# Kernel optimization log

Measured on AMD Instinct MI355X. Metric: run time of the kernel, lower is better.

Reference implementation:

```python
import jax, jax.numpy as jnp
import numpy as np

DIM = 1024
NUM_HEADS = 16
HEAD_DIM = DIM // NUM_HEADS
GATE_HID = DIM // 4


def setup_inputs() -> dict:
    key = jax.random.key(0)
    ks = jax.random.split(key, 16)
    B, S, D = 2, 2048, DIM
    sc = 1.0 / np.sqrt(D)
    inp = {
        "h": jax.random.normal(ks[0], (B, S, D), jnp.float32),
        "x": jax.random.normal(ks[1], (B, S, D), jnp.float32),
        # attention projections, stored (in, out) so y = x @ W + b
        "Wq": jax.random.normal(ks[2], (D, D), jnp.float32) * sc,
        "bq": jnp.zeros((D,), jnp.float32),
        "Wk": jax.random.normal(ks[3], (D, D), jnp.float32) * sc,
        "bk": jnp.zeros((D,), jnp.float32),
        "Wv": jax.random.normal(ks[4], (D, D), jnp.float32) * sc,
        "bv": jnp.zeros((D,), jnp.float32),
        "Wo": jax.random.normal(ks[5], (D, D), jnp.float32) * sc,
        "bo": jnp.zeros((D,), jnp.float32),
        # gating MLP: Linear(2D -> D//4) -> GELU -> Linear(D//4 -> D) -> sigmoid
        "Wg1": jax.random.normal(ks[6], (2 * D, GATE_HID), jnp.float32) * (1.0 / np.sqrt(2 * D)),
        "bg1": jnp.zeros((GATE_HID,), jnp.float32),
        "Wg2": jax.random.normal(ks[7], (GATE_HID, D), jnp.float32) * (1.0 / np.sqrt(GATE_HID)),
        "bg2": jnp.zeros((D,), jnp.float32),
    }
    return inp


def reference(h, x, Wq, bq, Wk, bk, Wv, bv, Wo, bo, Wg1, bg1, Wg2, bg2):
    B, S, D = h.shape
    # gated blend of latent h and input x
    gate_in = jnp.concatenate([h, x], axis=-1)                      # (B,S,2D)
    gate = jax.nn.sigmoid((jax.nn.gelu(gate_in @ Wg1 + bg1, approximate=False)) @ Wg2 + bg2)
    blended = gate * h + (1.0 - gate) * x                           # (B,S,D)
    # multi-head self-attention
    q = (blended @ Wq + bq).reshape(B, S, NUM_HEADS, HEAD_DIM)
    k = (blended @ Wk + bk).reshape(B, S, NUM_HEADS, HEAD_DIM)
    v = (blended @ Wv + bv).reshape(B, S, NUM_HEADS, HEAD_DIM)
    scale = 1.0 / np.sqrt(HEAD_DIM).astype(np.float32)
    scores = jnp.einsum('bqhd,bkhd->bhqk', q, k) * scale            # (B,H,S,S)
    attn = jax.nn.softmax(scores, axis=-1)
    out = jnp.einsum('bhqk,bkhd->bqhd', attn, v).reshape(B, S, D)
    return out @ Wo + bo
```

## Files before the change

### kernel.cpp

```cpp
#include <hip/hip_runtime.h>
#include <hip/hip_bf16.h>


typedef __attribute__((ext_vector_type(4))) unsigned int u32x4;
typedef __attribute__((ext_vector_type(2))) unsigned int u32x2;
typedef __attribute__((ext_vector_type(8))) short s16x8;
typedef __attribute__((ext_vector_type(8))) unsigned short u16x8;
typedef __attribute__((ext_vector_type(4))) unsigned short u16x4;
typedef __attribute__((ext_vector_type(4))) float f32x4;

#define QSCALE 0.18033688011112043f
#define FIXED_M 24.0f

__device__ __forceinline__ unsigned short f2bf(float f) {
    unsigned int i = __builtin_bit_cast(unsigned int, f) + 0x8000u;
    return (unsigned short)(i >> 16);
}
__device__ __forceinline__ unsigned int pack2bf(float a, float b) {
    unsigned int ia = __builtin_bit_cast(unsigned int, a) + 0x8000u;
    unsigned int ib = __builtin_bit_cast(unsigned int, b) + 0x8000u;
    return __builtin_amdgcn_perm(ib, ia, 0x07060302u);
}

__device__ __forceinline__ void gload16(const void* g, void* l) {
    __builtin_amdgcn_global_load_lds(
        (const __attribute__((address_space(1))) void*)g,
        (__attribute__((address_space(3))) void*)l, 16, 0, 0);
}

struct TEntry { const float* src; unsigned short* dst; int K; int N; };
struct TTable { TEntry e[6]; };

__global__ __launch_bounds__(256) void prep_all(
    TTable tt,
    const float* __restrict__ bq, const float* __restrict__ bk,
    const float* __restrict__ bv, float* __restrict__ bqkv)
{
    const int bid = (int)blockIdx.x;
    const int tid = threadIdx.x;
    if (bid < 3072) {
        const TEntry E = tt.e[bid >> 9];
        const int bx = bid & 511;
        const int ntn = E.N >> 5;
        if (bx >= (E.K >> 6) * ntn) return;
        const int n0 = (bx % ntn) * 32, k0 = (bx / ntn) * 64;
        __shared__ float tile[64][33];
        const int lnn = tid & 31, lkk = tid >> 5;
#pragma unroll
        for (int i = 0; i < 8; ++i)
            tile[lkk + i * 8][lnn] = E.src[(size_t)(k0 + lkk + i * 8) * E.N + n0 + lnn];
        __syncthreads();
        const int snn = tid >> 3, skk = (tid & 7) * 8;
        u16x8 o;
#pragma unroll
        for (int j = 0; j < 8; ++j) o[j] = f2bf(tile[skk + j][snn]);
        *reinterpret_cast<u16x8*>(&E.dst[(size_t)(n0 + snn) * E.K + k0 + skk]) = o;
        return;
    }
    const int i = (bid - 3072) * 256 + tid;
    if (i < 1024) bqkv[i] = bq[i];
    else if (i < 2048) bqkv[i] = bk[i - 1024];
    else if (i < 3072) bqkv[i] = bv[i - 2048];
}

__global__ __launch_bounds__(256) void transpose_v(
    const unsigned short* __restrict__ qkv, unsigned short* __restrict__ vt)
{
    __shared__ unsigned short t[64][65];
    const int st = blockIdx.x;
    const int bh = blockIdx.y;
    const int b = bh >> 4, h = bh & 15;
    const int tx = threadIdx.x & 63, ty = threadIdx.x >> 6;
    const int s0 = st * 64;
    const size_t base = (size_t)(b * 2048 + s0) * 3072 + 2048 + h * 64;
#pragma unroll
    for (int i = 0; i < 16; ++i)
        t[ty + i * 4][tx] = qkv[base + (size_t)(ty + i * 4) * 3072 + tx];
    __syncthreads();
    const size_t obase = (size_t)(bh * 64) * 2048 + s0;
#pragma unroll
    for (int i = 0; i < 16; ++i)
        vt[obase + (size_t)(ty + i * 4) * 2048 + tx] = t[tx][ty + i * 4];
}

enum { EPI_GELU = 1, EPI_BLEND = 2, EPI_F32 = 3, EPI_QKV = 4 };

template <int EPI>
__global__ __launch_bounds__(256, 3) void gemm_kernel(
    const unsigned short* __restrict__ A, int lda,
    const unsigned short* __restrict__ Bt, int ldb,
    const float* __restrict__ bias,
    void* __restrict__ Cv, int ldc, int K,
    const float* __restrict__ hb, const float* __restrict__ xb,
    int swzn, int ntn)
{
    __shared__ unsigned short Alds[2][128 * 32];
    __shared__ unsigned short Blds[2][128 * 32];

    const int tid = threadIdx.x;
    const int lane = tid & 63;
    const int w = tid >> 6;
    const int wr = w >> 1, wc = w & 1;
    int mt, nt;
    if (swzn > 0) {
        const int xcd = (int)blockIdx.x & 7, seq = (int)blockIdx.x >> 3;
        nt = xcd * swzn + seq % swzn;
        mt = seq / swzn;
    } else {
        nt = (int)blockIdx.x % ntn;
        mt = (int)blockIdx.x / ntn;
    }
    const int m0 = mt * 128, n0 = nt * 128;
    const int lrow = lane & 15, lko = (lane >> 4) * 8;

    const int grow = w * 32 + (lane >> 2);
    const int gk8 = (lane & 3) * 8;
    const unsigned short* ga0 = A + (size_t)(m0 + grow) * lda + gk8;
    const unsigned short* ga1 = ga0 + (size_t)16 * lda;
    const unsigned short* gb0 = Bt + (size_t)(n0 + grow) * ldb + gk8;
    const unsigned short* gb1 = gb0 + (size_t)16 * ldb;

    auto stage = [&](int buf, int k0) {
        unsigned short* la = &Alds[buf][w * 1024];
        unsigned short* lb = &Blds[buf][w * 1024];
        gload16(ga0 + k0, la);
        gload16(ga1 + k0, la + 512);
        gload16(gb0 + k0, lb);
        gload16(gb1 + k0, lb + 512);
    };

    f32x4 acc[4][4];
#pragma unroll
    for (int i = 0; i < 4; ++i)
#pragma unroll
        for (int j = 0; j < 4; ++j) acc[i][j] = (f32x4){0.f, 0.f, 0.f, 0.f};

    const int kks = K >> 5;
    stage(0, 0);
    __syncthreads();

    for (int t = 0; t < kks; ++t) {
        const int cur = t & 1;
        if (t + 1 < kks) stage(cur ^ 1, (t + 1) << 5);

        s16x8 af[4], bfr[4];
#pragma unroll
        for (int mi = 0; mi < 4; ++mi)
            af[mi] = *reinterpret_cast<const s16x8*>(&Alds[cur][(wr * 64 + mi * 16 + lrow) * 32 + lko]);
#pragma unroll
        for (int ni = 0; ni < 4; ++ni)
            bfr[ni] = *reinterpret_cast<const s16x8*>(&Blds[cur][(wc * 64 + ni * 16 + lrow) * 32 + lko]);
#pragma unroll
        for (int mi = 0; mi < 4; ++mi)
#pragma unroll
            for (int ni = 0; ni < 4; ++ni)
                acc[mi][ni] = __builtin_amdgcn_mfma_f32_16x16x32_bf16(af[mi], bfr[ni], acc[mi][ni], 0, 0, 0);

        __syncthreads();
    }

    const int rbase = m0 + wr * 64;
    const int cbase = n0 + wc * 64;
#pragma unroll
    for (int mi = 0; mi < 4; ++mi) {
#pragma unroll
        for (int j = 0; j < 4; ++j) {
            const int r = rbase + mi * 16 + (lane >> 4) * 4 + j;
#pragma unroll
            for (int ni = 0; ni < 4; ++ni) {
                const int c = cbase + ni * 16 + (lane & 15);
                float v = acc[mi][ni][j] + bias[c];
                if constexpr (EPI == EPI_GELU) {
                    float g = 0.5f * v * (1.f + erff(v * 0.70710678118654752f));
                    ((unsigned short*)Cv)[(size_t)r * ldc + c] = f2bf(g);
                } else if constexpr (EPI == EPI_BLEND) {
                    float gate = 1.f / (1.f + __expf(-v));
                    const size_t o = (size_t)r * ldc + c;
                    float bl = gate * hb[o] + (1.f - gate) * xb[o];
                    ((unsigned short*)Cv)[o] = f2bf(bl);
                } else if constexpr (EPI == EPI_QKV) {
                    const float scl = (c < 1024) ? QSCALE : 1.f;
                    ((unsigned short*)Cv)[(size_t)r * ldc + c] = f2bf(v * scl);
                } else {
                    ((float*)Cv)[(size_t)r * ldc + c] = v;
                }
            }
        }
    }
}

template <int EPI>
__global__ __launch_bounds__(256, 4) void gemm64_kernel(
    const unsigned short* __restrict__ A, int lda,
    const unsigned short* __restrict__ Bt, int ldb,
    const float* __restrict__ bias,
    void* __restrict__ Cv, int ldc, int K,
    const float* __restrict__ hb, const float* __restrict__ xb,
    int swzn)
{
    __shared__ unsigned short Alds[2][64 * 32];
    __shared__ unsigned short Blds[2][64 * 32];

    const int tid = threadIdx.x;
    const int lane = tid & 63;
    const int w = tid >> 6;
    const int wr = w >> 1, wc = w & 1;
    const int xcd = (int)blockIdx.x & 7, seq = (int)blockIdx.x >> 3;
    const int nt = xcd * swzn + seq % swzn;
    const int mt = seq / swzn;
    const int m0 = mt * 64, n0 = nt * 64;
    const int lrow = lane & 15, lko = (lane >> 4) * 8;

    const int grow = w * 16 + (lane >> 2);
    const int gk8 = (lane & 3) * 8;
    const unsigned short* ga = A + (size_t)(m0 + grow) * lda + gk8;
    const unsigned short* gb = Bt + (size_t)(n0 + grow) * ldb + gk8;

    auto stage = [&](int buf, int k0) {
        gload16(ga + k0, &Alds[buf][w * 512]);
        gload16(gb + k0, &Blds[buf][w * 512]);
    };

    f32x4 acc[2][2];
#pragma unroll
    for (int i = 0; i < 2; ++i)
#pragma unroll
        for (int j = 0; j < 2; ++j) acc[i][j] = (f32x4){0.f, 0.f, 0.f, 0.f};

    const int kks = K >> 5;
    stage(0, 0);
    __syncthreads();

    for (int t = 0; t < kks; ++t) {
        const int cur = t & 1;
        if (t + 1 < kks) stage(cur ^ 1, (t + 1) << 5);

        s16x8 af[2], bfr[2];
#pragma unroll
        for (int mi = 0; mi < 2; ++mi)
            af[mi] = *reinterpret_cast<const s16x8*>(&Alds[cur][(wr * 32 + mi * 16 + lrow) * 32 + lko]);
#pragma unroll
        for (int ni = 0; ni < 2; ++ni)
            bfr[ni] = *reinterpret_cast<const s16x8*>(&Blds[cur][(wc * 32 + ni * 16 + lrow) * 32 + lko]);
#pragma unroll
        for (int mi = 0; mi < 2; ++mi)
#pragma unroll
            for (int ni = 0; ni < 2; ++ni)
                acc[mi][ni] = __builtin_amdgcn_mfma_f32_16x16x32_bf16(af[mi], bfr[ni], acc[mi][ni], 0, 0, 0);

        __syncthreads();
    }

    const int rbase = m0 + wr * 32;
    const int cbase = n0 + wc * 32;
#pragma unroll
    for (int mi = 0; mi < 2; ++mi) {
#pragma unroll
        for (int j = 0; j < 4; ++j) {
            const int r = rbase + mi * 16 + (lane >> 4) * 4 + j;
#pragma unroll
            for (int ni = 0; ni < 2; ++ni) {
                const int c = cbase + ni * 16 + (lane & 15);
                float v = acc[mi][ni][j] + bias[c];
                if constexpr (EPI == EPI_BLEND) {
                    float gate = 1.f / (1.f + __expf(-v));
                    const size_t o = (size_t)r * ldc + c;
                    float bl = gate * hb[o] + (1.f - gate) * xb[o];
                    ((unsigned short*)Cv)[o] = f2bf(bl);
                } else {
                    ((float*)Cv)[(size_t)r * ldc + c] = v;
                }
            }
        }
    }
}

__global__ __launch_bounds__(256, 4) void gelu_partial(
    const float* __restrict__ h, const float* __restrict__ x,
    const unsigned short* __restrict__ Bt,
    float* __restrict__ partial)
{
    __shared__ unsigned short Alds[2][32 * 32];
    __shared__ unsigned short Blds[2][256 * 32];

    const int tid = threadIdx.x;
    const int lane = tid & 63;
    const int w = tid >> 6;
    const int mt = (int)blockIdx.x >> 2, ks = (int)blockIdx.x & 3;
    const int m0 = mt * 32, kbase = ks * 512;
    const int lrow = lane & 15, lko = (lane >> 4) * 8;

    const int arl = tid >> 3, ac4 = (tid & 7) * 4;
    const size_t arg = (size_t)(m0 + arl) * 1024;
    auto loadA = [&](int k0, f32x4& v) {
        v = *reinterpret_cast<const f32x4*>((k0 < 1024 ? h : x) + arg + (k0 & 1023) + ac4);
    };
    auto writeA = [&](int buf, const f32x4& v) {
        u32x2 p = {pack2bf(v[0], v[1]), pack2bf(v[2], v[3])};
        *reinterpret_cast<u32x2*>(&Alds[buf][arl * 32 + ac4]) = p;
    };

    const int brow = w * 64 + (lane >> 2);
    const int bk8 = (lane & 3) * 8;
    const unsigned short* gb = Bt + (size_t)brow * 2048 + kbase + bk8;
    auto stageB = [&](int buf, int k0) {
#pragma unroll
        for (int i = 0; i < 4; ++i)
            gload16(gb + (size_t)(i * 16) * 2048 + k0, &Blds[buf][(w * 64 + i * 16) * 32]);
    };

    f32x4 acc[2][4];
#pragma unroll
    for (int i = 0; i < 2; ++i)
#pragma unroll
        for (int j = 0; j < 4; ++j) acc[i][j] = (f32x4){0.f, 0.f, 0.f, 0.f};

    f32x4 areg;
    loadA(kbase, areg);
    stageB(0, 0);
    writeA(0, areg);
    __syncthreads();

    for (int t = 0; t < 16; ++t) {
        const int cur = t & 1;
        if (t + 1 < 16) {
            loadA(kbase + ((t + 1) << 5), areg);
            stageB(cur ^ 1, (t + 1) << 5);
        }

        s16x8 af[2], bfr[4];
#pragma unroll
        for (int mi = 0; mi < 2; ++mi)
            af[mi] = *reinterpret_cast<const s16x8*>(&Alds[cur][(mi * 16 + lrow) * 32 + lko]);
#pragma unroll
        for (int ni = 0; ni < 4; ++ni)
            bfr[ni] = *reinterpret_cast<const s16x8*>(&Blds[cur][(w * 64 + ni * 16 + lrow) * 32 + lko]);
#pragma unroll
        for (int mi = 0; mi < 2; ++mi)
#pragma unroll
            for (int ni = 0; ni < 4; ++ni)
                acc[mi][ni] = __builtin_amdgcn_mfma_f32_16x16x32_bf16(af[mi], bfr[ni], acc[mi][ni], 0, 0, 0);

        if (t + 1 < 16) writeA(cur ^ 1, areg);
        __syncthreads();
    }

    float* pbase = partial + (size_t)ks * 4096 * 256;
#pragma unroll
    for (int mi = 0; mi < 2; ++mi) {
#pragma unroll
        for (int j = 0; j < 4; ++j) {
            const int r = m0 + mi * 16 + (lane >> 4) * 4 + j;
#pragma unroll
            for (int ni = 0; ni < 4; ++ni) {
                const int c = w * 64 + ni * 16 + (lane & 15);
                pbase[(size_t)r * 256 + c] = acc[mi][ni][j];
            }
        }
    }
}

__global__ __launch_bounds__(256) void gelu_reduce(
    const float* __restrict__ partial, const float* __restrict__ bias,
    unsigned short* __restrict__ g1)
{
    const size_t idx = ((size_t)blockIdx.x * 256 + threadIdx.x) * 4;
    const int c = (int)(idx & 255);
    f32x4 s = *reinterpret_cast<const f32x4*>(partial + idx);
#pragma unroll
    for (int ks = 1; ks < 4; ++ks) {
        f32x4 p = *reinterpret_cast<const f32x4*>(partial + (size_t)ks * 4096 * 256 + idx);
        s[0] += p[0]; s[1] += p[1]; s[2] += p[2]; s[3] += p[3];
    }
    f32x4 bb = *reinterpret_cast<const f32x4*>(bias + c);
    u16x4 o;
#pragma unroll
    for (int j = 0; j < 4; ++j) {
        float v = s[j] + bb[j];
        o[j] = f2bf(0.5f * v * (1.f + erff(v * 0.70710678118654752f)));
    }
    *reinterpret_cast<u16x4*>(g1 + idx) = o;
}

#define ALD 72

__global__ __launch_bounds__(256, 3) void attn_kernel(
    const unsigned short* __restrict__ qkv,
    const unsigned short* __restrict__ vt,
    unsigned short* __restrict__ out)
{
    __shared__ unsigned short Klds[2][64 * 64];
    __shared__ unsigned short Vlds[2][64 * 64];
    __shared__ unsigned short Plds[2][4][16 * ALD];

    const int tid = threadIdx.x, lane = tid & 63, w = tid >> 6;
    const int xcd = (int)blockIdx.x & 7, seq = (int)blockIdx.x >> 3;
    const int bh = xcd * 4 + (seq & 3);
    const int qt = seq >> 2;
    const int b = bh >> 4, h = bh & 15;
    const int rb = b * 2048;
    const int lrow = lane & 15, g = lane >> 4, lko = g * 8;

    s16x8 qf[2][2];
#pragma unroll
    for (int qg = 0; qg < 2; ++qg) {
        const size_t qrow = (size_t)(rb + qt * 128 + w * 32 + qg * 16 + lrow) * 3072 + h * 64;
        qf[qg][0] = *reinterpret_cast<const s16x8*>(qkv + qrow + lko);
        qf[qg][1] = *reinterpret_cast<const s16x8*>(qkv + qrow + 32 + lko);
    }

    const int grow = w * 16 + (lane >> 3);
    const int gswz = ((lane & 7) ^ (lane >> 3)) * 8;
    const unsigned short* kgp = qkv + (size_t)(rb + grow) * 3072 + 1024 + h * 64 + gswz;
    const unsigned short* vgp = vt + (size_t)(bh * 64 + grow) * 2048 + gswz;

    auto stage = [&](int buf, int t0) {
        gload16(kgp + (size_t)t0 * 3072, &Klds[buf][w * 1024]);
        gload16(kgp + (size_t)(t0 + 8) * 3072, &Klds[buf][w * 1024 + 512]);
        gload16(vgp + t0, &Vlds[buf][w * 1024]);
        gload16(vgp + t0 + 8 * 2048, &Vlds[buf][w * 1024 + 512]);
    };

    const int cs0 = ((g) ^ (lrow & 7)) * 8;
    const int cs1 = ((4 + g) ^ (lrow & 7)) * 8;

    f32x4 acc0[4], acc1[4];
#pragma unroll
    for (int di = 0; di < 4; ++di) {
        acc0[di] = (f32x4){0.f, 0.f, 0.f, 0.f};
        acc1[di] = (f32x4){0.f, 0.f, 0.f, 0.f};
    }
    float lsum0 = 0.f, lsum1 = 0.f;

    unsigned short* pw0 = &Plds[0][w][0];
    unsigned short* pw1 = &Plds[1][w][0];
    s16x8 vf[2][4];

    stage(0, 0);
    __syncthreads();

    for (int t0 = 0; t0 < 2048; t0 += 64) {
        const int cur = (t0 >> 6) & 1;
        if (t0 + 64 < 2048) stage(cur ^ 1, t0 + 64);

        if (t0 > 0) {
            __builtin_amdgcn_s_setprio(1);
#pragma unroll
            for (int st = 0; st < 2; ++st) {
                s16x8 pf0 = *reinterpret_cast<const s16x8*>(&pw0[lrow * ALD + st * 32 + lko]);
#pragma unroll
                for (int di = 0; di < 4; ++di)
                    acc0[di] = __builtin_amdgcn_mfma_f32_16x16x32_bf16(vf[st][di], pf0, acc0[di], 0, 0, 0);
            }
#pragma unroll
            for (int st = 0; st < 2; ++st) {
                s16x8 pf1 = *reinterpret_cast<const s16x8*>(&pw1[lrow * ALD + st * 32 + lko]);
#pragma unroll
                for (int di = 0; di < 4; ++di)
                    acc1[di] = __builtin_amdgcn_mfma_f32_16x16x32_bf16(vf[st][di], pf1, acc1[di], 0, 0, 0);
            }
            __builtin_amdgcn_s_setprio(0);
        }

        s16x8 kf[4][2];
#pragma unroll
        for (int ni = 0; ni < 4; ++ni) {
            kf[ni][0] = *reinterpret_cast<const s16x8*>(&Klds[cur][(ni * 16 + lrow) * 64 + cs0]);
            kf[ni][1] = *reinterpret_cast<const s16x8*>(&Klds[cur][(ni * 16 + lrow) * 64 + cs1]);
        }

        f32x4 s0[4];
#pragma unroll
        for (int ni = 0; ni < 4; ++ni)
            s0[ni] = (f32x4){-FIXED_M, -FIXED_M, -FIXED_M, -FIXED_M};
        __builtin_amdgcn_s_setprio(1);
#pragma unroll
        for (int ni = 0; ni < 4; ++ni)
#pragma unroll
            for (int fi = 0; fi < 2; ++fi)
                s0[ni] = __builtin_amdgcn_mfma_f32_16x16x32_bf16(kf[ni][fi], qf[0][fi], s0[ni], 0, 0, 0);
        __builtin_amdgcn_s_setprio(0);

#pragma unroll
        for (int ni = 0; ni < 4; ++ni) {
            float p0 = __builtin_amdgcn_exp2f(s0[ni][0]);
            float p1 = __builtin_amdgcn_exp2f(s0[ni][1]);
            float p2 = __builtin_amdgcn_exp2f(s0[ni][2]);
            float p3 = __builtin_amdgcn_exp2f(s0[ni][3]);
            lsum0 += (p0 + p1) + (p2 + p3);
            u32x2 pk = {pack2bf(p0, p1), pack2bf(p2, p3)};
            *reinterpret_cast<u32x2*>(&pw0[lrow * ALD + ni * 16 + g * 4]) = pk;
        }

        f32x4 s1[4];
#pragma unroll
        for (int ni = 0; ni < 4; ++ni)
            s1[ni] = (f32x4){-FIXED_M, -FIXED_M, -FIXED_M, -FIXED_M};
        __builtin_amdgcn_s_setprio(1);
#pragma unroll
        for (int ni = 0; ni < 4; ++ni)
#pragma unroll
            for (int fi = 0; fi < 2; ++fi)
                s1[ni] = __builtin_amdgcn_mfma_f32_16x16x32_bf16(kf[ni][fi], qf[1][fi], s1[ni], 0, 0, 0);
        __builtin_amdgcn_s_setprio(0);

#pragma unroll
        for (int di = 0; di < 4; ++di) {
            vf[0][di] = *reinterpret_cast<const s16x8*>(&Vlds[cur][(di * 16 + lrow) * 64 + cs0]);
            vf[1][di] = *reinterpret_cast<const s16x8*>(&Vlds[cur][(di * 16 + lrow) * 64 + cs1]);
        }

#pragma unroll
        for (int ni = 0; ni < 4; ++ni) {
            float p0 = __builtin_amdgcn_exp2f(s1[ni][0]);
            float p1 = __builtin_amdgcn_exp2f(s1[ni][1]);
            float p2 = __builtin_amdgcn_exp2f(s1[ni][2]);
            float p3 = __builtin_amdgcn_exp2f(s1[ni][3]);
            lsum1 += (p0 + p1) + (p2 + p3);
            u32x2 pk = {pack2bf(p0, p1), pack2bf(p2, p3)};
            *reinterpret_cast<u32x2*>(&pw1[lrow * ALD + ni * 16 + g * 4]) = pk;
        }

        __syncthreads();
    }

#pragma unroll
    for (int st = 0; st < 2; ++st) {
        s16x8 pf0 = *reinterpret_cast<const s16x8*>(&pw0[lrow * ALD + st * 32 + lko]);
#pragma unroll
        for (int di = 0; di < 4; ++di)
            acc0[di] = __builtin_amdgcn_mfma_f32_16x16x32_bf16(vf[st][di], pf0, acc0[di], 0, 0, 0);
    }
#pragma unroll
    for (int st = 0; st < 2; ++st) {
        s16x8 pf1 = *reinterpret_cast<const s16x8*>(&pw1[lrow * ALD + st * 32 + lko]);
#pragma unroll
        for (int di = 0; di < 4; ++di)
            acc1[di] = __builtin_amdgcn_mfma_f32_16x16x32_bf16(vf[st][di], pf1, acc1[di], 0, 0, 0);
    }

    lsum0 += __shfl_xor(lsum0, 16);
    lsum0 += __shfl_xor(lsum0, 32);
    lsum1 += __shfl_xor(lsum1, 16);
    lsum1 += __shfl_xor(lsum1, 32);
    const float inv0 = 1.f / lsum0;
    const float inv1 = 1.f / lsum1;
    const size_t orow0 = (size_t)(rb + qt * 128 + w * 32 + lrow) * 1024 + h * 64;
    const size_t orow1 = orow0 + (size_t)16 * 1024;
#pragma unroll
    for (int di = 0; di < 4; ++di) {
        u32x2 ov0 = {pack2bf(acc0[di][0] * inv0, acc0[di][1] * inv0),
                     pack2bf(acc0[di][2] * inv0, acc0[di][3] * inv0)};
        *reinterpret_cast<u32x2*>(&out[orow0 + di * 16 + g * 4]) = ov0;
        u32x2 ov1 = {pack2bf(acc1[di][0] * inv1, acc1[di][1] * inv1),
                     pack2bf(acc1[di][2] * inv1, acc1[di][3] * inv1)};
        *reinterpret_cast<u32x2*>(&out[orow1 + di * 16 + g * 4]) = ov1;
    }
}

extern "C" void kernel_launch(void* const* d_in, const int* in_sizes, int n_in,
                              void* d_out, int out_size, void* d_ws, size_t ws_size,
                              hipStream_t stream)
{
    const float* h   = (const float*)d_in[0];
    const float* x   = (const float*)d_in[1];
    const float* Wq  = (const float*)d_in[2];
    const float* bq  = (const float*)d_in[3];
    const float* Wk  = (const float*)d_in[4];
    const float* bk  = (const float*)d_in[5];
    const float* Wv  = (const float*)d_in[6];
    const float* bv  = (const float*)d_in[7];
    const float* Wo  = (const float*)d_in[8];
    const float* bo  = (const float*)d_in[9];
    const float* Wg1 = (const float*)d_in[10];
    const float* bg1 = (const float*)d_in[11];
    const float* Wg2 = (const float*)d_in[12];
    const float* bg2 = (const float*)d_in[13];

    char* ws = (char*)d_ws;
    size_t off = 0;
    auto alloc = [&](size_t bytes) {
        void* p = ws + off;
        off += (bytes + 255) & ~(size_t)255;
        return p;
    };
    unsigned short* wg1T  = (unsigned short*)alloc((size_t)256 * 2048 * 2);
    unsigned short* wg2T  = (unsigned short*)alloc((size_t)1024 * 256 * 2);
    unsigned short* wqkvT = (unsigned short*)alloc((size_t)3072 * 1024 * 2);
    unsigned short* woT   = (unsigned short*)alloc((size_t)1024 * 1024 * 2);
    float*          bqkv  = (float*)alloc((size_t)3072 * 4);
    unsigned short* blend = (unsigned short*)alloc((size_t)4096 * 1024 * 2);
    unsigned short* attno = (unsigned short*)alloc((size_t)4096 * 1024 * 2);
    unsigned short* vtb   = (unsigned short*)alloc((size_t)32 * 64 * 2048 * 2);
    unsigned short* g1    = (unsigned short*)alloc((size_t)4096 * 256 * 2);
    unsigned short* qkv   = (unsigned short*)alloc((size_t)4096 * 3072 * 2);
    float* partial = (float*)qkv;
    (void)ws_size; (void)in_sizes; (void)n_in; (void)out_size;

    TTable tt;
    tt.e[0] = {Wg1, wg1T, 2048, 256};
    tt.e[1] = {Wg2, wg2T, 256, 1024};
    tt.e[2] = {Wq, wqkvT, 1024, 1024};
    tt.e[3] = {Wk, wqkvT + (size_t)1024 * 1024, 1024, 1024};
    tt.e[4] = {Wv, wqkvT + (size_t)2048 * 1024, 1024, 1024};
    tt.e[5] = {Wo, woT, 1024, 1024};
    prep_all<<<3072 + 12, 256, 0, stream>>>(tt, bq, bk, bv, bqkv);

    gelu_partial<<<512, 256, 0, stream>>>(h, x, wg1T, partial);
    gelu_reduce<<<1024, 256, 0, stream>>>(partial, bg1, g1);
    gemm64_kernel<EPI_BLEND><<<1024, 256, 0, stream>>>(
        g1, 256, wg2T, 256, bg2, blend, 1024, 256, h, x, 2);

    gemm_kernel<EPI_QKV><<<768, 256, 0, stream>>>(
        blend, 1024, wqkvT, 1024, bqkv, qkv, 3072, 1024, nullptr, nullptr, 3, 24);

    transpose_v<<<dim3(32, 32), 256, 0, stream>>>(qkv, vtb);

    attn_kernel<<<512, 256, 0, stream>>>(qkv, vtb, attno);

    gemm64_kernel<EPI_F32><<<1024, 256, 0, stream>>>(
        attno, 1024, woT, 1024, bo, (float*)d_out, 1024, 1024, nullptr, nullptr, 2);
}
```

Measured before the change: 147.8 us.

## Double query rows per attention block to amortize K/V tile loads

```diff
diff --git a/kernel.cpp b/kernel.cpp
--- a/kernel.cpp
+++ b/kernel.cpp
@@ -384,14 +384,14 @@
 
 #define ALD 72
 
-__global__ __launch_bounds__(256, 3) void attn_kernel(
+__global__ __launch_bounds__(256, 1) void attn_kernel(
     const unsigned short* __restrict__ qkv,
     const unsigned short* __restrict__ vt,
     unsigned short* __restrict__ out)
 {
     __shared__ unsigned short Klds[2][64 * 64];
     __shared__ unsigned short Vlds[2][64 * 64];
-    __shared__ unsigned short Plds[2][4][16 * ALD];
+    __shared__ unsigned short Plds[4][4][16 * ALD];
 
     const int tid = threadIdx.x, lane = tid & 63, w = tid >> 6;
     const int xcd = (int)blockIdx.x & 7, seq = (int)blockIdx.x >> 3;
@@ -401,10 +401,10 @@
     const int rb = b * 2048;
     const int lrow = lane & 15, g = lane >> 4, lko = g * 8;
 
-    s16x8 qf[2][2];
-#pragma unroll
-    for (int qg = 0; qg < 2; ++qg) {
-        const size_t qrow = (size_t)(rb + qt * 128 + w * 32 + qg * 16 + lrow) * 3072 + h * 64;
+    s16x8 qf[4][2];
+#pragma unroll
+    for (int qg = 0; qg < 4; ++qg) {
+        const size_t qrow = (size_t)(rb + qt * 256 + w * 64 + qg * 16 + lrow) * 3072 + h * 64;
         qf[qg][0] = *reinterpret_cast<const s16x8*>(qkv + qrow + lko);
         qf[qg][1] = *reinterpret_cast<const s16x8*>(qkv + qrow + 32 + lko);
     }
@@ -424,16 +424,17 @@
     const int cs0 = ((g) ^ (lrow & 7)) * 8;
     const int cs1 = ((4 + g) ^ (lrow & 7)) * 8;
 
-    f32x4 acc0[4], acc1[4];
-#pragma unroll
-    for (int di = 0; di < 4; ++di) {
-        acc0[di] = (f32x4){0.f, 0.f, 0.f, 0.f};
-        acc1[di] = (f32x4){0.f, 0.f, 0.f, 0.f};
-    }
-    float lsum0 = 0.f, lsum1 = 0.f;
+    f32x4 acc[4][4];
+#pragma unroll
+    for (int qg = 0; qg < 4; ++qg)
+#pragma unroll
+        for (int di = 0; di < 4; ++di) acc[qg][di] = (f32x4){0.f, 0.f, 0.f, 0.f};
+    float lsum[4] = {0.f, 0.f, 0.f, 0.f};
 
     unsigned short* pw0 = &Plds[0][w][0];
     unsigned short* pw1 = &Plds[1][w][0];
+    unsigned short* pw2 = &Plds[2][w][0];
+    unsigned short* pw3 = &Plds[3][w][0];
     s16x8 vf[2][4];
 
     stage(0, 0);
@@ -447,17 +448,31 @@
             __builtin_amdgcn_s_setprio(1);
 #pragma unroll
             for (int st = 0; st < 2; ++st) {
-                s16x8 pf0 = *reinterpret_cast<const s16x8*>(&pw0[lrow * ALD + st * 32 + lko]);
+                s16x8 pf = *reinterpret_cast<const s16x8*>(&pw0[lrow * ALD + st * 32 + lko]);
 #pragma unroll
                 for (int di = 0; di < 4; ++di)
-                    acc0[di] = __builtin_amdgcn_mfma_f32_16x16x32_bf16(vf[st][di], pf0, acc0[di], 0, 0, 0);
+                    acc[0][di] = __builtin_amdgcn_mfma_f32_16x16x32_bf16(vf[st][di], pf, acc[0][di], 0, 0, 0);
             }
 #pragma unroll
             for (int st = 0; st < 2; ++st) {
-                s16x8 pf1 = *reinterpret_cast<const s16x8*>(&pw1[lrow * ALD + st * 32 + lko]);
+                s16x8 pf = *reinterpret_cast<const s16x8*>(&pw1[lrow * ALD + st * 32 + lko]);
 #pragma unroll
                 for (int di = 0; di < 4; ++di)
-                    acc1[di] = __builtin_amdgcn_mfma_f32_16x16x32_bf16(vf[st][di], pf1, acc1[di], 0, 0, 0);
+                    acc[1][di] = __builtin_amdgcn_mfma_f32_16x16x32_bf16(vf[st][di], pf, acc[1][di], 0, 0, 0);
+            }
+#pragma unroll
+            for (int st = 0; st < 2; ++st) {
+                s16x8 pf = *reinterpret_cast<const s16x8*>(&pw2[lrow * ALD + st * 32 + lko]);
+#pragma unroll
+                for (int di = 0; di < 4; ++di)
+                    acc[2][di] = __builtin_amdgcn_mfma_f32_16x16x32_bf16(vf[st][di], pf, acc[2][di], 0, 0, 0);
+            }
+#pragma unroll
+            for (int st = 0; st < 2; ++st) {
+                s16x8 pf = *reinterpret_cast<const s16x8*>(&pw3[lrow * ALD + st * 32 + lko]);
+#pragma unroll
+                for (int di = 0; di < 4; ++di)
+                    acc[3][di] = __builtin_amdgcn_mfma_f32_16x16x32_bf16(vf[st][di], pf, acc[3][di], 0, 0, 0);
             }
             __builtin_amdgcn_s_setprio(0);
         }
@@ -469,40 +484,34 @@
             kf[ni][1] = *reinterpret_cast<const s16x8*>(&Klds[cur][(ni * 16 + lrow) * 64 + cs1]);
         }
 
-        f32x4 s0[4];
-#pragma unroll
-        for (int ni = 0; ni < 4; ++ni)
-            s0[ni] = (f32x4){-FIXED_M, -FIXED_M, -FIXED_M, -FIXED_M};
-        __builtin_amdgcn_s_setprio(1);
-#pragma unroll
-        for (int ni = 0; ni < 4; ++ni)
-#pragma unroll
-            for (int fi = 0; fi < 2; ++fi)
-                s0[ni] = __builtin_amdgcn_mfma_f32_16x16x32_bf16(kf[ni][fi], qf[0][fi], s0[ni], 0, 0, 0);
-        __builtin_amdgcn_s_setprio(0);
-
-#pragma unroll
-        for (int ni = 0; ni < 4; ++ni) {
-            float p0 = __builtin_amdgcn_exp2f(s0[ni][0]);
-            float p1 = __builtin_amdgcn_exp2f(s0[ni][1]);
-            float p2 = __builtin_amdgcn_exp2f(s0[ni][2]);
-            float p3 = __builtin_amdgcn_exp2f(s0[ni][3]);
-            lsum0 += (p0 + p1) + (p2 + p3);
-            u32x2 pk = {pack2bf(p0, p1), pack2bf(p2, p3)};
-            *reinterpret_cast<u32x2*>(&pw0[lrow * ALD + ni * 16 + g * 4]) = pk;
-        }
-
-        f32x4 s1[4];
-#pragma unroll
-        for (int ni = 0; ni < 4; ++ni)
-            s1[ni] = (f32x4){-FIXED_M, -FIXED_M, -FIXED_M, -FIXED_M};
-        __builtin_amdgcn_s_setprio(1);
-#pragma unroll
-        for (int ni = 0; ni < 4; ++ni)
-#pragma unroll
-            for (int fi = 0; fi < 2; ++fi)
-                s1[ni] = __builtin_amdgcn_mfma_f32_16x16x32_bf16(kf[ni][fi], qf[1][fi], s1[ni], 0, 0, 0);
-        __builtin_amdgcn_s_setprio(0);
+#pragma unroll
+        for (int qg = 0; qg < 4; ++qg) {
+            f32x4 s[4];
+#pragma unroll
+            for (int ni = 0; ni < 4; ++ni)
+                s[ni] = (f32x4){-FIXED_M, -FIXED_M, -FIXED_M, -FIXED_M};
+            __builtin_amdgcn_s_setprio(1);
+#pragma unroll
+            for (int ni = 0; ni < 4; ++ni)
+#pragma unroll
+                for (int fi = 0; fi < 2; ++fi)
+                    s[ni] = __builtin_amdgcn_mfma_f32_16x16x32_bf16(kf[ni][fi], qf[qg][fi], s[ni], 0, 0, 0);
+            __builtin_amdgcn_s_setprio(0);
+
+            unsigned short* pw = (qg == 0) ? pw0 : (qg == 1) ? pw1 : (qg == 2) ? pw2 : pw3;
+            float ls = 0.f;
+#pragma unroll
+            for (int ni = 0; ni < 4; ++ni) {
+                float p0 = __builtin_amdgcn_exp2f(s[ni][0]);
+                float p1 = __builtin_amdgcn_exp2f(s[ni][1]);
+                float p2 = __builtin_amdgcn_exp2f(s[ni][2]);
+                float p3 = __builtin_amdgcn_exp2f(s[ni][3]);
+                ls += (p0 + p1) + (p2 + p3);
+                u32x2 pk = {pack2bf(p0, p1), pack2bf(p2, p3)};
+                *reinterpret_cast<u32x2*>(&pw[lrow * ALD + ni * 16 + g * 4]) = pk;
+            }
+            lsum[qg] += ls;
+        }
 
 #pragma unroll
         for (int di = 0; di < 4; ++di) {
@@ -510,51 +519,51 @@
             vf[1][di] = *reinterpret_cast<const s16x8*>(&Vlds[cur][(di * 16 + lrow) * 64 + cs1]);
         }
 
-#pragma unroll
-        for (int ni = 0; ni < 4; ++ni) {
-            float p0 = __builtin_amdgcn_exp2f(s1[ni][0]);
-            float p1 = __builtin_amdgcn_exp2f(s1[ni][1]);
-            float p2 = __builtin_amdgcn_exp2f(s1[ni][2]);
-            float p3 = __builtin_amdgcn_exp2f(s1[ni][3]);
-            lsum1 += (p0 + p1) + (p2 + p3);
-            u32x2 pk = {pack2bf(p0, p1), pack2bf(p2, p3)};
-            *reinterpret_cast<u32x2*>(&pw1[lrow * ALD + ni * 16 + g * 4]) = pk;
-        }
-
         __syncthreads();
     }
 
 #pragma unroll
     for (int st = 0; st < 2; ++st) {
-        s16x8 pf0 = *reinterpret_cast<const s16x8*>(&pw0[lrow * ALD + st * 32 + lko]);
+        s16x8 pf = *reinterpret_cast<const s16x8*>(&pw0[lrow * ALD + st * 32 + lko]);
 #pragma unroll
         for (int di = 0; di < 4; ++di)
-            acc0[di] = __builtin_amdgcn_mfma_f32_16x16x32_bf16(vf[st][di], pf0, acc0[di], 0, 0, 0);
+            acc[0][di] = __builtin_amdgcn_mfma_f32_16x16x32_bf16(vf[st][di], pf, acc[0][di], 0, 0, 0);
     }
 #pragma unroll
     for (int st = 0; st < 2; ++st) {
-        s16x8 pf1 = *reinterpret_cast<const s16x8*>(&pw1[lrow * ALD + st * 32 + lko]);
+        s16x8 pf = *reinterpret_cast<const s16x8*>(&pw1[lrow * ALD + st * 32 + lko]);
 #pragma unroll
         for (int di = 0; di < 4; ++di)
-            acc1[di] = __builtin_amdgcn_mfma_f32_16x16x32_bf16(vf[st][di], pf1, acc1[di], 0, 0, 0);
-    }
-
-    lsum0 += __shfl_xor(lsum0, 16);
-    lsum0 += __shfl_xor(lsum0, 32);
-    lsum1 += __shfl_xor(lsum1, 16);
-    lsum1 += __shfl_xor(lsum1, 32);
-    const float inv0 = 1.f / lsum0;
-    const float inv1 = 1.f / lsum1;
-    const size_t orow0 = (size_t)(rb + qt * 128 + w * 32 + lrow) * 1024 + h * 64;
-    const size_t orow1 = orow0 + (size_t)16 * 1024;
-#pragma unroll
-    for (int di = 0; di < 4; ++di) {
-        u32x2 ov0 = {pack2bf(acc0[di][0] * inv0, acc0[di][1] * inv0),
-                     pack2bf(acc0[di][2] * inv0, acc0[di][3] * inv0)};
-        *reinterpret_cast<u32x2*>(&out[orow0 + di * 16 + g * 4]) = ov0;
-        u32x2 ov1 = {pack2bf(acc1[di][0] * inv1, acc1[di][1] * inv1),
-                     pack2bf(acc1[di][2] * inv1, acc1[di][3] * inv1)};
-        *reinterpret_cast<u32x2*>(&out[orow1 + di * 16 + g * 4]) = ov1;
+            acc[1][di] = __builtin_amdgcn_mfma_f32_16x16x32_bf16(vf[st][di], pf, acc[1][di], 0, 0, 0);
+    }
+#pragma unroll
+    for (int st = 0; st < 2; ++st) {
+        s16x8 pf = *reinterpret_cast<const s16x8*>(&pw2[lrow * ALD + st * 32 + lko]);
+#pragma unroll
+        for (int di = 0; di < 4; ++di)
+            acc[2][di] = __builtin_amdgcn_mfma_f32_16x16x32_bf16(vf[st][di], pf, acc[2][di], 0, 0, 0);
+    }
+#pragma unroll
+    for (int st = 0; st < 2; ++st) {
+        s16x8 pf = *reinterpret_cast<const s16x8*>(&pw3[lrow * ALD + st * 32 + lko]);
+#pragma unroll
+        for (int di = 0; di < 4; ++di)
+            acc[3][di] = __builtin_amdgcn_mfma_f32_16x16x32_bf16(vf[st][di], pf, acc[3][di], 0, 0, 0);
+    }
+
+#pragma unroll
+    for (int qg = 0; qg < 4; ++qg) {
+        float ls = lsum[qg];
+        ls += __shfl_xor(ls, 16);
+        ls += __shfl_xor(ls, 32);
+        const float inv = 1.f / ls;
+        const size_t orow = (size_t)(rb + qt * 256 + w * 64 + qg * 16 + lrow) * 1024 + h * 64;
+#pragma unroll
+        for (int di = 0; di < 4; ++di) {
+            u32x2 ov = {pack2bf(acc[qg][di][0] * inv, acc[qg][di][1] * inv),
+                        pack2bf(acc[qg][di][2] * inv, acc[qg][di][3] * inv)};
+            *reinterpret_cast<u32x2*>(&out[orow + di * 16 + g * 4]) = ov;
+        }
     }
 }
 
@@ -616,7 +625,7 @@
 
     transpose_v<<<dim3(32, 32), 256, 0, stream>>>(qkv, vtb);
 
-    attn_kernel<<<512, 256, 0, stream>>>(qkv, vtb, attno);
+    attn_kernel<<<256, 256, 0, stream>>>(qkv, vtb, attno);
 
     gemm64_kernel<EPI_F32><<<1024, 256, 0, stream>>>(
         attno, 1024, woT, 1024, bo, (float*)d_out, 1024, 1024, nullptr, nullptr, 2);
```

New measurement: 164.0 us. 1.11x slower.

## Fuse V projection with transpose into dedicated GEMM writing V^T directly

Applied to the files above, without the earlier changes.

```diff
diff --git a/kernel.cpp b/kernel.cpp
--- a/kernel.cpp
+++ b/kernel.cpp
@@ -61,26 +61,6 @@
     if (i < 1024) bqkv[i] = bq[i];
     else if (i < 2048) bqkv[i] = bk[i - 1024];
     else if (i < 3072) bqkv[i] = bv[i - 2048];
-}
-
-__global__ __launch_bounds__(256) void transpose_v(
-    const unsigned short* __restrict__ qkv, unsigned short* __restrict__ vt)
-{
-    __shared__ unsigned short t[64][65];
-    const int st = blockIdx.x;
-    const int bh = blockIdx.y;
-    const int b = bh >> 4, h = bh & 15;
-    const int tx = threadIdx.x & 63, ty = threadIdx.x >> 6;
-    const int s0 = st * 64;
-    const size_t base = (size_t)(b * 2048 + s0) * 3072 + 2048 + h * 64;
-#pragma unroll
-    for (int i = 0; i < 16; ++i)
-        t[ty + i * 4][tx] = qkv[base + (size_t)(ty + i * 4) * 3072 + tx];
-    __syncthreads();
-    const size_t obase = (size_t)(bh * 64) * 2048 + s0;
-#pragma unroll
-    for (int i = 0; i < 16; ++i)
-        vt[obase + (size_t)(ty + i * 4) * 2048 + tx] = t[tx][ty + i * 4];
 }
 
 enum { EPI_GELU = 1, EPI_BLEND = 2, EPI_F32 = 3, EPI_QKV = 4 };
@@ -275,6 +255,91 @@
     }
 }
 
+__global__ __launch_bounds__(256, 4) void gemm_vt(
+    const unsigned short* __restrict__ A,
+    const unsigned short* __restrict__ Bt,
+    const float* __restrict__ bias,
+    unsigned short* __restrict__ vt)
+{
+    __shared__ unsigned short Alds[2][64 * 32];
+    __shared__ unsigned short Blds[2][64 * 32];
+    __shared__ unsigned short Clds[64][72];
+
+    const int tid = threadIdx.x;
+    const int lane = tid & 63;
+    const int w = tid >> 6;
+    const int wr = w >> 1, wc = w & 1;
+    const int xcd = (int)blockIdx.x & 7, seq = (int)blockIdx.x >> 3;
+    const int nt = xcd * 2 + (seq & 1);
+    const int mt = seq >> 1;
+    const int m0 = mt * 64, n0 = nt * 64;
+    const int lrow = lane & 15, lko = (lane >> 4) * 8;
+
+    const int grow = w * 16 + (lane >> 2);
+    const int gk8 = (lane & 3) * 8;
+    const unsigned short* ga = A + (size_t)(m0 + grow) * 1024 + gk8;
+    const unsigned short* gb = Bt + (size_t)(n0 + grow) * 1024 + gk8;
+
+    auto stage = [&](int buf, int k0) {
+        gload16(ga + k0, &Alds[buf][w * 512]);
+        gload16(gb + k0, &Blds[buf][w * 512]);
+    };
+
+    f32x4 acc[2][2];
+#pragma unroll
+    for (int i = 0; i < 2; ++i)
+#pragma unroll
+        for (int j = 0; j < 2; ++j) acc[i][j] = (f32x4){0.f, 0.f, 0.f, 0.f};
+
+    stage(0, 0);
+    __syncthreads();
+
+    for (int t = 0; t < 32; ++t) {
+        const int cur = t & 1;
+        if (t + 1 < 32) stage(cur ^ 1, (t + 1) << 5);
+
+        s16x8 af[2], bfr[2];
+#pragma unroll
+        for (int mi = 0; mi < 2; ++mi)
+            af[mi] = *reinterpret_cast<const s16x8*>(&Alds[cur][(wr * 32 + mi * 16 + lrow) * 32 + lko]);
+#pragma unroll
+        for (int ni = 0; ni < 2; ++ni)
+            bfr[ni] = *reinterpret_cast<const s16x8*>(&Blds[cur][(wc * 32 + ni * 16 + lrow) * 32 + lko]);
+#pragma unroll
+        for (int mi = 0; mi < 2; ++mi)
+#pragma unroll
+            for (int ni = 0; ni < 2; ++ni)
+                acc[mi][ni] = __builtin_amdgcn_mfma_f32_16x16x32_bf16(af[mi], bfr[ni], acc[mi][ni], 0, 0, 0);
+
+        __syncthreads();
+    }
+
+#pragma unroll
+    for (int mi = 0; mi < 2; ++mi) {
+#pragma unroll
+        for (int j = 0; j < 4; ++j) {
+            const int rl = wr * 32 + mi * 16 + (lane >> 4) * 4 + j;
+#pragma unroll
+            for (int ni = 0; ni < 2; ++ni) {
+                const int cl = wc * 32 + ni * 16 + (lane & 15);
+                Clds[rl][cl] = f2bf(acc[mi][ni][j] + bias[n0 + cl]);
+            }
+        }
+    }
+    __syncthreads();
+
+    const int b = m0 >> 11, s0 = m0 & 2047;
+    const int d = tid & 63, ch = tid >> 6;
+    u16x8 o0, o1;
+#pragma unroll
+    for (int i = 0; i < 8; ++i) o0[i] = Clds[ch * 16 + i][d];
+#pragma unroll
+    for (int i = 0; i < 8; ++i) o1[i] = Clds[ch * 16 + 8 + i][d];
+    unsigned short* dst = vt + ((size_t)((b * 16 + nt) * 64 + d)) * 2048 + s0 + ch * 16;
+    *reinterpret_cast<u16x8*>(dst) = o0;
+    *reinterpret_cast<u16x8*>(dst + 8) = o1;
+}
+
 __global__ __launch_bounds__(256, 4) void gelu_partial(
     const float* __restrict__ h, const float* __restrict__ x,
     const unsigned short* __restrict__ Bt,
@@ -385,7 +450,7 @@
 #define ALD 72
 
 __global__ __launch_bounds__(256, 3) void attn_kernel(
-    const unsigned short* __restrict__ qkv,
+    const unsigned short* __restrict__ qk,
     const unsigned short* __restrict__ vt,
     unsigned short* __restrict__ out)
 {
@@ -404,19 +469,19 @@
     s16x8 qf[2][2];
 #pragma unroll
     for (int qg = 0; qg < 2; ++qg) {
-        const size_t qrow = (size_t)(rb + qt * 128 + w * 32 + qg * 16 + lrow) * 3072 + h * 64;
-        qf[qg][0] = *reinterpret_cast<const s16x8*>(qkv + qrow + lko);
-        qf[qg][1] = *reinterpret_cast<const s16x8*>(qkv + qrow + 32 + lko);
+        const size_t qrow = (size_t)(rb + qt * 128 + w * 32 + qg * 16 + lrow) * 2048 + h * 64;
+        qf[qg][0] = *reinterpret_cast<const s16x8*>(qk + qrow + lko);
+        qf[qg][1] = *reinterpret_cast<const s16x8*>(qk + qrow + 32 + lko);
     }
 
     const int grow = w * 16 + (lane >> 3);
     const int gswz = ((lane & 7) ^ (lane >> 3)) * 8;
-    const unsigned short* kgp = qkv + (size_t)(rb + grow) * 3072 + 1024 + h * 64 + gswz;
+    const unsigned short* kgp = qk + (size_t)(rb + grow) * 2048 + 1024 + h * 64 + gswz;
     const unsigned short* vgp = vt + (size_t)(bh * 64 + grow) * 2048 + gswz;
 
     auto stage = [&](int buf, int t0) {
-        gload16(kgp + (size_t)t0 * 3072, &Klds[buf][w * 1024]);
-        gload16(kgp + (size_t)(t0 + 8) * 3072, &Klds[buf][w * 1024 + 512]);
+        gload16(kgp + (size_t)t0 * 2048, &Klds[buf][w * 1024]);
+        gload16(kgp + (size_t)(t0 + 8) * 2048, &Klds[buf][w * 1024 + 512]);
         gload16(vgp + t0, &Vlds[buf][w * 1024]);
         gload16(vgp + t0 + 8 * 2048, &Vlds[buf][w * 1024 + 512]);
     };
@@ -593,8 +658,8 @@
     unsigned short* attno = (unsigned short*)alloc((size_t)4096 * 1024 * 2);
     unsigned short* vtb   = (unsigned short*)alloc((size_t)32 * 64 * 2048 * 2);
     unsigned short* g1    = (unsigned short*)alloc((size_t)4096 * 256 * 2);
-    unsigned short* qkv   = (unsigned short*)alloc((size_t)4096 * 3072 * 2);
-    float* partial = (float*)qkv;
+    unsigned short* qk    = (unsigned short*)alloc((size_t)4096 * 2048 * 2);
+    float* partial = (float*)qk;
     (void)ws_size; (void)in_sizes; (void)n_in; (void)out_size;
 
     TTable tt;
@@ -611,12 +676,13 @@
     gemm64_kernel<EPI_BLEND><<<1024, 256, 0, stream>>>(
         g1, 256, wg2T, 256, bg2, blend, 1024, 256, h, x, 2);
 
-    gemm_kernel<EPI_QKV><<<768, 256, 0, stream>>>(
-        blend, 1024, wqkvT, 1024, bqkv, qkv, 3072, 1024, nullptr, nullptr, 3, 24);
-
-    transpose_v<<<dim3(32, 32), 256, 0, stream>>>(qkv, vtb);
-
-    attn_kernel<<<512, 256, 0, stream>>>(qkv, vtb, attno);
+    gemm_kernel<EPI_QKV><<<512, 256, 0, stream>>>(
+        blend, 1024, wqkvT, 1024, bqkv, qk, 2048, 1024, nullptr, nullptr, 2, 16);
+
+    gemm_vt<<<1024, 256, 0, stream>>>(
+        blend, wqkvT + (size_t)2048 * 1024, bqkv + 2048, vtb);
+
+    attn_kernel<<<512, 256, 0, stream>>>(qk, vtb, attno);
 
     gemm64_kernel<EPI_F32><<<1024, 256, 0, stream>>>(
         attno, 1024, woT, 1024, bo, (float*)d_out, 1024, 1024, nullptr, nullptr, 2);
```

Measured after the change: 160.3 us. 1.08x slower.
